# Kernel optimization log

Measured on AMD Instinct MI355X. Metric: run time of the kernel, lower is better.

The kernel has to match this reference:

```python
import jax, jax.numpy as jnp
import numpy as np

N, D, NBINS, NUM_IDS = 8192, 256, 64, 512
MAX_DIST = 2.0  # initial +/- histogram range from __init__ (max_dist default)
EPS_DIST = 1e-12
EPS_HIST = 1e-6


def setup_inputs() -> dict:
    key = jax.random.key(0)
    kx, kt = jax.random.split(key)
    x = jax.random.normal(kx, (N, D), dtype=jnp.float32)
    targets = jax.random.randint(kt, (N,), 0, NUM_IDS, dtype=jnp.int64)
    histogram = jnp.ones((NBINS,), dtype=jnp.float32)  # buffer initial state
    return {"x": x, "targets": targets, "histogram": histogram}


def reference(x, targets, histogram):
    n = x.shape[0]
    nbins = histogram.shape[0]
    # pairwise euclidean distances: [n, n]
    sq = jnp.sum(x * x, axis=1)
    dist = jnp.sqrt(jnp.clip(sq[:, None] + sq[None, :] - 2.0 * (x @ x.T), EPS_DIST, None))
    mask = targets[:, None] == targets[None, :]
    neg_inf = jnp.array(-jnp.inf, dtype=dist.dtype)
    pos_inf = jnp.array(jnp.inf, dtype=dist.dtype)
    pos_dist = jnp.max(jnp.where(mask, dist, neg_inf), axis=1)  # hardest positive per row
    neg_dist = jnp.min(jnp.where(mask, pos_inf, dist), axis=1)  # hardest negative per row
    hist_val = pos_dist - neg_dist
    # _compute_histogram: widen range by batch extremes (torch uses .item() on detached values)
    hv = jax.lax.stop_gradient(hist_val)
    max_val = jnp.maximum(jnp.max(hv), MAX_DIST)
    min_val = jnp.minimum(jnp.min(hv), -MAX_DIST)
    bin_width = (max_val - min_val) / (nbins - 1)
    lo = jnp.floor((hv - min_val) / bin_width).astype(jnp.int32)
    hi = jnp.clip(lo + 1, 0, nbins - 1)
    alpha = 1.0 - (hv - min_val - lo.astype(hv.dtype) * bin_width) / bin_width
    hist = jnp.zeros((nbins,), dtype=hv.dtype).at[lo].add(alpha).at[hi].add(1.0 - alpha)
    hist = hist / (jnp.sum(hist) + EPS_HIST)
    # first call: _stats_initialized is False -> momentum = 1.0, new buffer = hist
    new_histogram = hist
    pdf = new_histogram / jnp.sum(new_histogram)
    cdf = jnp.cumsum(pdf)
    bin_idx = jnp.floor((hv - min_val) / bin_width).astype(jnp.int32)
    weight = cdf[bin_idx]  # detached weighting (built entirely from stop_gradient values)
    loss = -jnp.mean(neg_dist * weight) + jnp.mean(pos_dist * weight)
    return loss
```

## Files before the change

### kernel.cpp

```cpp
#include <hip/hip_runtime.h>
#include <math.h>

#define Nn 8192
#define Dd 256
#define NBINS 64
#define NSPLIT 8

typedef __attribute__((ext_vector_type(8))) short short8;
typedef __attribute__((ext_vector_type(4))) float f32x4;

#define GLOAD16(g, l)                                                        \
  __builtin_amdgcn_global_load_lds(                                          \
      (const __attribute__((address_space(1))) void*)(g),                    \
      (__attribute__((address_space(3))) void*)(l), 16, 0, 0)

static __device__ __forceinline__ unsigned short f2bf(float f) {
  unsigned int u = __float_as_uint(f);
  u = (u + 0x7fffu + ((u >> 16) & 1u)) >> 16;
  return (unsigned short)u;
}
static __device__ __forceinline__ unsigned int enc_ord(float f) {
  unsigned int u = __float_as_uint(f);
  return (u & 0x80000000u) ? ~u : (u | 0x80000000u);
}
static __device__ __forceinline__ float dec_ord(unsigned int u) {
  unsigned int b2 = (u & 0x80000000u) ? (u ^ 0x80000000u) : ~u;
  return __uint_as_float(b2);
}

__global__ __launch_bounds__(256) void prep_kernel(const float* __restrict__ x,
                                                   const int* __restrict__ lab,
                                                   unsigned short* __restrict__ xb,
                                                   float2* __restrict__ sqlab,
                                                   unsigned int* __restrict__ pos2,
                                                   unsigned int* __restrict__ neg2,
                                                   unsigned int* __restrict__ gmm,
                                                   float* __restrict__ ghist,
                                                   float* __restrict__ ghsum,
                                                   unsigned int* __restrict__ cnt) {
  const int w = threadIdx.x >> 6;
  const int lane = threadIdx.x & 63;
  const int row = blockIdx.x * 4 + w;
  const float4 v = *(const float4*)(x + (size_t)row * Dd + lane * 4);
  ushort4 b;
  b.x = f2bf(v.x); b.y = f2bf(v.y); b.z = f2bf(v.z); b.w = f2bf(v.w);
  *(ushort4*)(xb + (size_t)row * Dd + lane * 4) = b;
  float s = v.x * v.x + v.y * v.y + v.z * v.z + v.w * v.w;
#pragma unroll
  for (int off = 32; off >= 1; off >>= 1) s += __shfl_xor(s, off);
  if (lane == 0) {
    sqlab[row] = make_float2(s, __int_as_float(lab[row]));
    pos2[row] = 0x007fffffu;
    neg2[row] = 0xff800000u;
  }
  if (blockIdx.x == 0 && threadIdx.x < NBINS) {
    ghist[threadIdx.x] = 0.0f;
    ghsum[threadIdx.x] = 0.0f;
    if (threadIdx.x == 0) { gmm[0] = 0x007fffffu; gmm[1] = 0xff800000u; cnt[0] = 0u; }
  }
}

static __device__ __forceinline__ void stage_a(const unsigned short* __restrict__ xb,
                                               int r0, int hh, unsigned short* buf, int t) {
#pragma unroll
  for (int i = 0; i < 8; ++i) {
    const int c = i * 256 + t;
    const int col = c >> 4;
    const int kq = (c & 15) ^ (col & 15);
    GLOAD16(xb + (size_t)(r0 + col) * Dd + hh * 128 + kq * 8, buf + (size_t)c * 8);
  }
}
static __device__ __forceinline__ void stage_b(const unsigned short* __restrict__ xb,
                                               int c0, int hh, unsigned short* buf, int t) {
#pragma unroll
  for (int i = 0; i < 4; ++i) {
    const int c = i * 256 + t;
    const int col = c >> 4;
    const int kq = (c & 15) ^ (col & 15);
    GLOAD16(xb + (size_t)(c0 + col) * Dd + hh * 128 + kq * 8, buf + (size_t)c * 8);
  }
}

__global__ __launch_bounds__(256, 2) void pairwise_kernel(const unsigned short* __restrict__ xb,
                                                          const float2* __restrict__ sqlab,
                                                          unsigned int* __restrict__ pos2,
                                                          unsigned int* __restrict__ neg2) {
  __shared__ __align__(16) unsigned short Us[4096 * 8];
  __shared__ __align__(16) float2 sl_s[1024];
  __shared__ int lab_s[128];

  const int t = threadIdx.x;
  const int lane = t & 63;
  const int w = t >> 6;
  const int wr = w >> 1;
  const int wc = w & 1;
  const int c_l = lane & 15;
  const int kq_l = lane >> 4;
  const int rows0 = blockIdx.x * 128;
  const int cbase = blockIdx.y * (Nn / NSPLIT);

  stage_a(xb, rows0, 0, Us, t);
  stage_a(xb, rows0, 1, Us + 2048 * 8, t);
#pragma unroll
  for (int i = 0; i < 4; ++i) sl_s[i * 256 + t] = sqlab[cbase + i * 256 + t];
  if (t < 128) lab_s[t] = __float_as_int(sqlab[rows0 + t].y);
  __syncthreads();

  const short8* Uv = (const short8*)Us;
  short8 af[32];
#pragma unroll
  for (int k2 = 0; k2 < 8; ++k2)
#pragma unroll
    for (int m = 0; m < 4; ++m) {
      const int kqf = k2 * 4 + kq_l;
      const int rl = wr * 64 + m * 16 + c_l;
      af[k2 * 4 + m] = Uv[(kqf >> 4) * 2048 + rl * 16 + ((kqf & 15) ^ (rl & 15))];
    }
  int labp[8];
#pragma unroll
  for (int m = 0; m < 4; ++m)
#pragma unroll
    for (int pp = 0; pp < 2; ++pp) {
      const int r0 = wr * 64 + m * 16 + kq_l * 4 + 2 * pp;
      labp[m * 2 + pp] = (lab_s[r0] & 0xffff) | (lab_s[r0 + 1] << 16);
    }
  __syncthreads();

  unsigned short* const Bs0 = Us;
  unsigned short* const Bs1 = Us + 2048 * 8;

  stage_b(xb, cbase, 0, Bs0, t);
  stage_b(xb, cbase, 1, Bs0 + 1024 * 8, t);

  const int cc0 = wc * 32 + c_l;
  const int cc1 = wc * 32 + 16 + c_l;
  const int x0 = cc0 & 15, x1 = cc1 & 15;
  float pmax[16], nmin[16];
#pragma unroll
  for (int i = 0; i < 16; ++i) { pmax[i] = -INFINITY; nmin[i] = INFINITY; }

#pragma unroll 1
  for (int ct2 = 0; ct2 < 8; ++ct2) {
#pragma unroll
    for (int half = 0; half < 2; ++half) {
      const int ct = 2 * ct2 + half;
      const unsigned short* const bufR = half ? Bs1 : Bs0;
      unsigned short* const bufW = half ? Bs0 : Bs1;

      __syncthreads();
      if (ct < 15) {
        stage_b(xb, cbase + (ct + 1) * 64, 0, bufW, t);
        stage_b(xb, cbase + (ct + 1) * 64, 1, bufW + 1024 * 8, t);
      }

      f32x4 acc[4][2];
#pragma unroll
      for (int m = 0; m < 4; ++m)
#pragma unroll
        for (int n = 0; n < 2; ++n) acc[m][n] = (f32x4){0.f, 0.f, 0.f, 0.f};

      const short8* const Bv0 = (const short8*)bufR;
      const short8* const Bv1 = (const short8*)(bufR + 1024 * 8);
#pragma unroll
      for (int ks = 0; ks < 8; ++ks) {
        const short8* const B = (ks < 4) ? Bv0 : Bv1;
        const int o = (ks & 3) * 4 + kq_l;
        const short8 bf0 = B[cc0 * 16 + (o ^ x0)];
        const short8 bf1 = B[cc1 * 16 + (o ^ x1)];
#pragma unroll
        for (int m = 0; m < 4; ++m) {
          acc[m][0] = __builtin_amdgcn_mfma_f32_16x16x32_bf16(af[ks * 4 + m], bf0, acc[m][0], 0, 0, 0);
          acc[m][1] = __builtin_amdgcn_mfma_f32_16x16x32_bf16(af[ks * 4 + m], bf1, acc[m][1], 0, 0, 0);
        }
      }

      const float2 sl0 = sl_s[ct * 64 + cc0];
      const float2 sl1 = sl_s[ct * 64 + cc1];
      const int lc0 = __float_as_int(sl0.y);
      const int lc1 = __float_as_int(sl1.y);
#pragma unroll
      for (int idx = 0; idx < 16; ++idx) {
        const int m = idx >> 2, q = idx & 3;
        const int lr = (labp[idx >> 1] >> ((idx & 1) * 16)) & 0xffff;
        const float g0 = fmaf(-2.0f, acc[m][0][q], sl0.x);
        const float g1 = fmaf(-2.0f, acc[m][1][q], sl1.x);
        const bool s0 = (lr == lc0), s1 = (lr == lc1);
        const float gp0 = s0 ? g0 : -INFINITY, gp1 = s1 ? g1 : -INFINITY;
        const float gn0 = s0 ? INFINITY : g0,  gn1 = s1 ? INFINITY : g1;
        pmax[idx] = fmaxf(fmaxf(pmax[idx], gp0), gp1);
        nmin[idx] = fminf(fminf(nmin[idx], gn0), gn1);
      }
    }
  }

#pragma unroll
  for (int i = 0; i < 16; ++i) {
    float p = pmax[i], nn2 = nmin[i];
#pragma unroll
    for (int off = 1; off < 16; off <<= 1) {
      p = fmaxf(p, __shfl_xor(p, off));
      nn2 = fminf(nn2, __shfl_xor(nn2, off));
    }
    if (c_l == 0) {
      const int rowg = rows0 + wr * 64 + (i >> 2) * 16 + kq_l * 4 + (i & 3);
      atomicMax(&pos2[rowg], enc_ord(p));
      atomicMin(&neg2[rowg], enc_ord(nn2));
    }
  }
}

__global__ __launch_bounds__(512) void finalize_a_kernel(const float2* __restrict__ sqlab,
                                                         const unsigned int* __restrict__ pos2,
                                                         const unsigned int* __restrict__ neg2,
                                                         float* __restrict__ hv_g,
                                                         unsigned int* __restrict__ gmm) {
  const int i = blockIdx.x * 512 + threadIdx.x;
  const int lane = threadIdx.x & 63;
  const float s = sqlab[i].x;
  const float p2 = fmaxf(s + dec_ord(pos2[i]), 1e-12f);
  const float n2 = fmaxf(s + dec_ord(neg2[i]), 1e-12f);
  const float hv = sqrtf(p2) - sqrtf(n2);
  hv_g[i] = hv;
  float lmax = hv, lmin = hv;
#pragma unroll
  for (int off = 32; off >= 1; off >>= 1) {
    lmax = fmaxf(lmax, __shfl_xor(lmax, off));
    lmin = fminf(lmin, __shfl_xor(lmin, off));
  }
  if (lane == 0) {
    atomicMax(&gmm[0], enc_ord(lmax));
    atomicMin(&gmm[1], enc_ord(lmin));
  }
}

__global__ __launch_bounds__(512) void finalize_b_kernel(const float* __restrict__ hv_g,
                                                         const unsigned int* __restrict__ gmm,
                                                         float* __restrict__ ghist,
                                                         float* __restrict__ ghsum,
                                                         unsigned int* __restrict__ cnt,
                                                         float* __restrict__ out) {
  __shared__ float hist_s[NBINS];
  __shared__ float hsum_s[NBINS];
  __shared__ unsigned int s_last;
  const int t = threadIdx.x;
  if (t < NBINS) { hist_s[t] = 0.0f; hsum_s[t] = 0.0f; }
  const float maxv = fmaxf(dec_ord(gmm[0]), 2.0f);
  const float minv = fminf(dec_ord(gmm[1]), -2.0f);
  const float bw = (maxv - minv) / (float)(NBINS - 1);
  __syncthreads();

  const int i = blockIdx.x * 512 + t;
  const float hv = hv_g[i];
  int lo = (int)floorf((hv - minv) / bw);
  lo = min(max(lo, 0), NBINS - 1);
  const int hi = min(lo + 1, NBINS - 1);
  const float alpha = 1.0f - (hv - minv - (float)lo * bw) / bw;
  atomicAdd(&hist_s[lo], alpha);
  atomicAdd(&hist_s[hi], 1.0f - alpha);
  atomicAdd(&hsum_s[lo], hv);
  __syncthreads();

  if (t < NBINS) {
    atomicAdd(&ghist[t], hist_s[t]);
    atomicAdd(&ghsum[t], hsum_s[t]);
  }
  __threadfence();
  if (t == 0) s_last = atomicAdd(cnt, 1u);
  __syncthreads();
  if (s_last != (unsigned int)(gridDim.x - 1)) return;

  if (t < NBINS) {
    const float h = __hip_atomic_load(&ghist[t], __ATOMIC_RELAXED, __HIP_MEMORY_SCOPE_AGENT);
    const float hs = __hip_atomic_load(&ghsum[t], __ATOMIC_RELAXED, __HIP_MEMORY_SCOPE_AGENT);
    float total = h;
#pragma unroll
    for (int off = 32; off >= 1; off >>= 1) total += __shfl_xor(total, off);
    const float hn = h / (total + 1e-6f);
    float s2 = hn;
#pragma unroll
    for (int off = 32; off >= 1; off >>= 1) s2 += __shfl_xor(s2, off);
    const float pdf = hn / s2;
    float c = pdf;
#pragma unroll
    for (int off = 1; off < 64; off <<= 1) {
      const float u = __shfl_up(c, off);
      if (t >= off) c += u;
    }
    float acc = c * hs;
#pragma unroll
    for (int off = 32; off >= 1; off >>= 1) acc += __shfl_xor(acc, off);
    if (t == 0) out[0] = acc / (float)Nn;
  }
}

extern "C" void kernel_launch(void* const* d_in, const int* in_sizes, int n_in,
                              void* d_out, int out_size, void* d_ws, size_t ws_size,
                              hipStream_t stream) {
  const float* x = (const float*)d_in[0];
  const int* targets = (const int*)d_in[1];
  float* out = (float*)d_out;

  char* p = (char*)d_ws;
  unsigned short* xb = (unsigned short*)p;  p += (size_t)Nn * Dd * 2;
  float2* sqlab = (float2*)p;               p += (size_t)Nn * 8;
  unsigned int* pos2 = (unsigned int*)p;    p += (size_t)Nn * 4;
  unsigned int* neg2 = (unsigned int*)p;    p += (size_t)Nn * 4;
  float* hv_g = (float*)p;                  p += (size_t)Nn * 4;
  unsigned int* gmm = (unsigned int*)p;     p += 64;
  float* ghist = (float*)p;                 p += NBINS * 4;
  float* ghsum = (float*)p;                 p += NBINS * 4;
  unsigned int* cnt = (unsigned int*)p;

  prep_kernel<<<Nn / 4, 256, 0, stream>>>(x, targets, xb, sqlab, pos2, neg2, gmm, ghist, ghsum, cnt);
  pairwise_kernel<<<dim3(Nn / 128, NSPLIT), 256, 0, stream>>>(xb, sqlab, pos2, neg2);
  finalize_a_kernel<<<Nn / 512, 512, 0, stream>>>(sqlab, pos2, neg2, hv_g, gmm);
  finalize_b_kernel<<<Nn / 512, 512, 0, stream>>>(hv_g, gmm, ghist, ghsum, cnt, out);
}
```

Measured before the change: 64.86 us.

## Software-pipeline epilogue of second column tile behind next tile's MFMAs

Splits the per-tile MFMA accumulation into two column halves and defers the mask/min-max epilogue of the second half to the next iteration, so that epilogue VALU work can overlap with MFMA execution. The first half's epilogue still runs right after its MFMAs, and a final drain handles the last deferred tile. This adds carried accumulator state and may raise register pressure under the 2-wave launch bound.

```diff
diff --git a/kernel.cpp b/kernel.cpp
--- a/kernel.cpp
+++ b/kernel.cpp
@@ -81,6 +81,20 @@
   }
 }
 
+static __device__ __forceinline__ void epi_col(const f32x4 (&a)[4], float sc, int lc,
+                                               const int (&labp)[8],
+                                               float (&pmax)[16], float (&nmin)[16]) {
+#pragma unroll
+  for (int idx = 0; idx < 16; ++idx) {
+    const int m = idx >> 2, q = idx & 3;
+    const int lr = (labp[idx >> 1] >> ((idx & 1) * 16)) & 0xffff;
+    const float g = fmaf(-2.0f, a[m][q], sc);
+    const bool sm = (lr == lc);
+    pmax[idx] = fmaxf(pmax[idx], sm ? g : -INFINITY);
+    nmin[idx] = fminf(nmin[idx], sm ? INFINITY : g);
+  }
+}
+
 __global__ __launch_bounds__(256, 2) void pairwise_kernel(const unsigned short* __restrict__ xb,
                                                           const float2* __restrict__ sqlab,
                                                           unsigned int* __restrict__ pos2,
@@ -139,6 +153,9 @@
 #pragma unroll
   for (int i = 0; i < 16; ++i) { pmax[i] = -INFINITY; nmin[i] = INFINITY; }
 
+  f32x4 a0[4];
+  f32x4 a1p[4];
+
 #pragma unroll 1
   for (int ct2 = 0; ct2 < 8; ++ct2) {
 #pragma unroll
@@ -153,44 +170,46 @@
         stage_b(xb, cbase + (ct + 1) * 64, 1, bufW + 1024 * 8, t);
       }
 
-      f32x4 acc[4][2];
-#pragma unroll
-      for (int m = 0; m < 4; ++m)
-#pragma unroll
-        for (int n = 0; n < 2; ++n) acc[m][n] = (f32x4){0.f, 0.f, 0.f, 0.f};
+      if (ct > 0) {
+        const float2 slp = sl_s[(ct - 1) * 64 + cc1];
+        epi_col(a1p, slp.x, __float_as_int(slp.y), labp, pmax, nmin);
+      }
+
+#pragma unroll
+      for (int m = 0; m < 4; ++m) {
+        a0[m] = (f32x4){0.f, 0.f, 0.f, 0.f};
+        a1p[m] = (f32x4){0.f, 0.f, 0.f, 0.f};
+      }
 
       const short8* const Bv0 = (const short8*)bufR;
       const short8* const Bv1 = (const short8*)(bufR + 1024 * 8);
+
 #pragma unroll
       for (int ks = 0; ks < 8; ++ks) {
         const short8* const B = (ks < 4) ? Bv0 : Bv1;
         const int o = (ks & 3) * 4 + kq_l;
         const short8 bf0 = B[cc0 * 16 + (o ^ x0)];
+#pragma unroll
+        for (int m = 0; m < 4; ++m)
+          a0[m] = __builtin_amdgcn_mfma_f32_16x16x32_bf16(af[ks * 4 + m], bf0, a0[m], 0, 0, 0);
+      }
+#pragma unroll
+      for (int ks = 0; ks < 8; ++ks) {
+        const short8* const B = (ks < 4) ? Bv0 : Bv1;
+        const int o = (ks & 3) * 4 + kq_l;
         const short8 bf1 = B[cc1 * 16 + (o ^ x1)];
 #pragma unroll
-        for (int m = 0; m < 4; ++m) {
-          acc[m][0] = __builtin_amdgcn_mfma_f32_16x16x32_bf16(af[ks * 4 + m], bf0, acc[m][0], 0, 0, 0);
-          acc[m][1] = __builtin_amdgcn_mfma_f32_16x16x32_bf16(af[ks * 4 + m], bf1, acc[m][1], 0, 0, 0);
-        }
+        for (int m = 0; m < 4; ++m)
+          a1p[m] = __builtin_amdgcn_mfma_f32_16x16x32_bf16(af[ks * 4 + m], bf1, a1p[m], 0, 0, 0);
       }
 
       const float2 sl0 = sl_s[ct * 64 + cc0];
-      const float2 sl1 = sl_s[ct * 64 + cc1];
-      const int lc0 = __float_as_int(sl0.y);
-      const int lc1 = __float_as_int(sl1.y);
-#pragma unroll
-      for (int idx = 0; idx < 16; ++idx) {
-        const int m = idx >> 2, q = idx & 3;
-        const int lr = (labp[idx >> 1] >> ((idx & 1) * 16)) & 0xffff;
-        const float g0 = fmaf(-2.0f, acc[m][0][q], sl0.x);
-        const float g1 = fmaf(-2.0f, acc[m][1][q], sl1.x);
-        const bool s0 = (lr == lc0), s1 = (lr == lc1);
-        const float gp0 = s0 ? g0 : -INFINITY, gp1 = s1 ? g1 : -INFINITY;
-        const float gn0 = s0 ? INFINITY : g0,  gn1 = s1 ? INFINITY : g1;
-        pmax[idx] = fmaxf(fmaxf(pmax[idx], gp0), gp1);
-        nmin[idx] = fminf(fminf(nmin[idx], gn0), gn1);
-      }
-    }
+      epi_col(a0, sl0.x, __float_as_int(sl0.y), labp, pmax, nmin);
+    }
+  }
+  {
+    const float2 slp = sl_s[15 * 64 + cc1];
+    epi_col(a1p, slp.x, __float_as_int(slp.y), labp, pmax, nmin);
   }
 
 #pragma unroll
```

After: 86.49 us. 1.33x slower.
